# Optimization experiments

Measured on AMD Instinct MI355X. Metric: run time of the kernel, lower is better.

The kernel has to match this reference:

```python
import jax, jax.numpy as jnp
import numpy as np

N_NODES = 100000
LATENT_DIM = 8
SAMPLE_SIZE = 8192
N_EDGES = 1000000
EPS = 1e-6


def setup_inputs() -> dict:
    key = jax.random.key(0)
    k1, k2, k3, k4, k5 = jax.random.split(key, 5)
    latent_Z = jax.random.normal(k1, (N_NODES, LATENT_DIM), dtype=jnp.float32)
    alpha = jax.random.normal(k2, (1,), dtype=jnp.float32)
    sample_idx = jax.random.randint(k3, (SAMPLE_SIZE,), 0, N_NODES, dtype=jnp.int64)
    sparse_sample_i = jax.random.randint(k4, (N_EDGES,), 0, N_NODES, dtype=jnp.int64)
    sparse_sample_j = jax.random.randint(k5, (N_EDGES,), 0, N_NODES, dtype=jnp.int64)
    return {"latent_Z": latent_Z, "alpha": alpha, "sample_idx": sample_idx,
            "sparse_sample_i": sparse_sample_i, "sparse_sample_j": sparse_sample_j}


def reference(latent_Z, alpha, sample_idx, sparse_sample_i, sparse_sample_j):
    # --- dense non-edge term over the sampled subgraph ---
    Zs = latent_Z[sample_idx]                              # [S, D]
    diff = Zs[:, None, :] - Zs[None, :, :] + EPS           # [S, S, D]
    dist = jnp.sqrt(jnp.sum(diff * diff, axis=-1))         # [S, S]
    mat = jnp.exp(-dist)                                   # [S, S]
    # original uses exp(ones) vectors in the matmul-with-ones trick -> factor e^2
    ones_exp_sq = jnp.exp(jnp.float32(1.0)) ** 2
    offdiag_sum = jnp.sum(mat) - jnp.sum(jnp.diagonal(mat))
    z_pdist1 = jnp.exp(alpha[0]) * 0.5 * ones_exp_sq * offdiag_sum
    # --- sparse positive-edge term ---
    ed = latent_Z[sparse_sample_i] - latent_Z[sparse_sample_j] + EPS  # [E, D]
    edist = jnp.sqrt(jnp.sum(ed * ed, axis=-1))                        # [E]
    z_pdist2 = jnp.sum(-edist + alpha[0])
    return z_pdist2 - z_pdist1
```

## Files before the change

kernel.cpp:

```cpp
#include <hip/hip_runtime.h>
#include <hip/hip_bf16.h>
#include <math.h>

#define NNODES   100000
#define S        8192
#define D        8
#define EPSF     1e-6f
#define LOG2E    1.442695040888963f
#define EPS_S    (LOG2E * EPSF)
#define NT2      256

#define ZBS_OFF  0
#define U_OFF    131104
#define V_OFF    163872
#define ZB_OFF   196640
#define BK_OFF   1796736

#define NSBLK    256
#define NDBLK    1024
#define NWPP     32
#define ZROW     8192

typedef __attribute__((ext_vector_type(8)))  short short8_t;
typedef __attribute__((ext_vector_type(16))) float f32x16;

__device__ __forceinline__ float block_reduce_f(float v, float* sm) {
    #pragma unroll
    for (int off = 32; off > 0; off >>= 1) v += __shfl_down(v, off, 64);
    int lane = threadIdx.x & 63, wid = threadIdx.x >> 6;
    if (lane == 0) sm[wid] = v;
    __syncthreads();
    float s = 0.f;
    if (threadIdx.x == 0) {
        for (int w = 0; w < 4; ++w) s += sm[w];
    }
    return s;
}

__global__ __launch_bounds__(256) void gather_kernel(const float* __restrict__ Z,
                                                     const int* __restrict__ idx,
                                                     ushort* __restrict__ zbs,
                                                     float* __restrict__ u,
                                                     float* __restrict__ v,
                                                     ushort* __restrict__ zb16,
                                                     char* __restrict__ buckets) {
    int gid = blockIdx.x * 256 + threadIdx.x;

    if (blockIdx.x == 0 && threadIdx.x < 161) {
        *(double*)(buckets + threadIdx.x * 128) = 0.0;
    }
    if (blockIdx.x == 0 && threadIdx.x == 200) {
        short8_t zz = { 0,0,0,0,0,0,0,0 };
        *(short8_t*)(zbs + (size_t)ZROW * 8) = zz;
    }

    if (gid < S) {
        int n = idx[gid];
        const float4* zp = (const float4*)(Z + (size_t)n * D);
        float4 a = zp[0], b = zp[1];
        float z[8] = { a.x, a.y, a.z, a.w, b.x, b.y, b.z, b.w };
        float ss = 0.f;
        short8_t h;
        #pragma unroll
        for (int k = 0; k < 8; ++k) {
            float zs = LOG2E * z[k];
            __hip_bfloat16 hb = __float2bfloat16(zs);
            float hf = __bfloat162float(hb);
            ss = fmaf(hf, hf, ss);
            h[k] = (short)__builtin_bit_cast(unsigned short, hb);
        }
        *(short8_t*)(zbs + (size_t)gid * 8) = h;
        u[gid] = ss + 8.f * EPS_S * EPS_S;
        v[gid] = ss;
    }

    if (gid < NNODES) {
        const float4* zp = (const float4*)(Z + (size_t)gid * D);
        float4 a = zp[0], b = zp[1];
        float z[8] = { a.x, a.y, a.z, a.w, b.x, b.y, b.z, b.w };
        short8_t o;
        #pragma unroll
        for (int k = 0; k < 8; ++k) {
            __hip_bfloat16 bb = __float2bfloat16(z[k]);
            o[k] = (short)__builtin_bit_cast(unsigned short, bb);
        }
        *(short8_t*)(zb16 + (size_t)gid * 8) = o;
    }
}

#define UNPACK8(u4, f)                                        \
    f[0] = __uint_as_float(u4.x << 16);                       \
    f[1] = __uint_as_float(u4.x & 0xffff0000u);               \
    f[2] = __uint_as_float(u4.y << 16);                       \
    f[3] = __uint_as_float(u4.y & 0xffff0000u);               \
    f[4] = __uint_as_float(u4.z << 16);                       \
    f[5] = __uint_as_float(u4.z & 0xffff0000u);               \
    f[6] = __uint_as_float(u4.w << 16);                       \
    f[7] = __uint_as_float(u4.w & 0xffff0000u);

__device__ __forceinline__ float edge_dist8(const uint4* __restrict__ zb,
                                            int4 ia0, int4 ia1, int4 ib0, int4 ib1) {
    int aidx[8] = { ia0.x, ia0.y, ia0.z, ia0.w, ia1.x, ia1.y, ia1.z, ia1.w };
    int bidx[8] = { ib0.x, ib0.y, ib0.z, ib0.w, ib1.x, ib1.y, ib1.z, ib1.w };
    uint4 ua[8], ub[8];
    #pragma unroll
    for (int q = 0; q < 8; ++q) { ua[q] = zb[aidx[q]]; ub[q] = zb[bidx[q]]; }
    float acc = 0.f;
    #pragma unroll
    for (int q = 0; q < 8; ++q) {
        float fa[8], fb[8];
        UNPACK8(ua[q], fa);
        UNPACK8(ub[q], fb);
        float s2 = 0.f;
        #pragma unroll
        for (int k = 0; k < 8; ++k) {
            float d = fa[k] - fb[k] + EPSF;
            s2 = fmaf(d, d, s2);
        }
        acc += __builtin_amdgcn_sqrtf(s2);
    }
    return acc;
}

__device__ __forceinline__ void dense_sweep32(const ushort* __restrict__ zbs,
                                              const float* __restrict__ v,
                                              short8_t afrag, const float4* u4,
                                              int ti, int tj0, int cnt, int c31, int g,
                                              float& ax, float& ay, float& az, float& aw) {
    const ushort* bp = zbs + (size_t)(g ? ZROW : (tj0 * 32 + c31)) * 8;
    size_t step = g ? 0 : 256;
    const float* vp = v + tj0 * 32 + c31;
    short8_t bnext = *(const short8_t*)bp;
    float    vnext = vp[0];
    #pragma unroll 4
    for (int t = 0; t < cnt; ++t) {
        short8_t bc = bnext;
        float    vtc = vnext;
        if (t + 1 < cnt) {
            bnext = *(const short8_t*)(bp + (size_t)(t + 1) * step);
            vnext = vp[(t + 1) * 32];
        }
        float w = (tj0 + t == ti) ? 1.f : 2.f;
        f32x16 c = { 0.f, 0.f, 0.f, 0.f, 0.f, 0.f, 0.f, 0.f,
                     0.f, 0.f, 0.f, 0.f, 0.f, 0.f, 0.f, 0.f };
        c = __builtin_amdgcn_mfma_f32_32x32x16_bf16(afrag, bc, c, 0, 0, 0);
        #pragma unroll
        for (int q = 0; q < 4; ++q) {
            float s0 = u4[q].x + vtc, s1 = u4[q].y + vtc;
            float s2 = u4[q].z + vtc, s3 = u4[q].w + vtc;
            float d0 = fmaf(c[4*q+0], -2.f, s0);
            float d1 = fmaf(c[4*q+1], -2.f, s1);
            float d2 = fmaf(c[4*q+2], -2.f, s2);
            float d3 = fmaf(c[4*q+3], -2.f, s3);
            ax = fmaf(w, __builtin_amdgcn_exp2f(-__builtin_amdgcn_sqrtf(__builtin_fabsf(d0))), ax);
            ay = fmaf(w, __builtin_amdgcn_exp2f(-__builtin_amdgcn_sqrtf(__builtin_fabsf(d1))), ay);
            az = fmaf(w, __builtin_amdgcn_exp2f(-__builtin_amdgcn_sqrtf(__builtin_fabsf(d2))), az);
            aw = fmaf(w, __builtin_amdgcn_exp2f(-__builtin_amdgcn_sqrtf(__builtin_fabsf(d3))), aw);
        }
    }
}

__global__ __launch_bounds__(256) void fused_kernel(
        const ushort* __restrict__ zbs, const float* __restrict__ u,
        const float* __restrict__ v, const ushort* __restrict__ zb16,
        const int* __restrict__ ei, const int* __restrict__ ej, int ne,
        const float* __restrict__ alpha, char* __restrict__ buckets,
        float* __restrict__ out) {
    __shared__ float red[4];
    __shared__ unsigned composeFlag;
    int tid = threadIdx.x, bx = blockIdx.x;
    float s;

    if (bx < NSBLK) {
        const uint4* zb = (const uint4*)zb16;
        const int4* ei4 = (const int4*)ei;
        const int4* ej4 = (const int4*)ej;
        float acc = 0.f;
        int nchunk = ne >> 3;
        int stride = NSBLK * 256;
        int c = bx * 256 + tid;
        if (c < nchunk) {
            int4 ia0 = ei4[2*c], ia1 = ei4[2*c+1];
            int4 ib0 = ej4[2*c], ib1 = ej4[2*c+1];
            while (true) {
                int cn = c + stride;
                bool more = cn < nchunk;
                int4 na0, na1, nb0, nb1;
                if (more) {
                    na0 = ei4[2*cn]; na1 = ei4[2*cn+1];
                    nb0 = ej4[2*cn]; nb1 = ej4[2*cn+1];
                }
                acc += edge_dist8(zb, ia0, ia1, ib0, ib1);
                if (!more) break;
                ia0 = na0; ia1 = na1; ib0 = nb0; ib1 = nb1; c = cn;
            }
        }
        for (int e = (nchunk << 3) + bx * 256 + tid; e < ne; e += stride) {
            uint4 ua = zb[ei[e]];
            uint4 ub = zb[ej[e]];
            float fa[8], fb[8];
            UNPACK8(ua, fa);
            UNPACK8(ub, fb);
            float s2 = 0.f;
            #pragma unroll
            for (int k = 0; k < 8; ++k) {
                float d = fa[k] - fb[k] + EPSF;
                s2 = fmaf(d, d, s2);
            }
            acc += __builtin_amdgcn_sqrtf(s2);
        }
        s = block_reduce_f(acc, red);
    } else {
        int dbx  = bx - NSBLK;
        int wave = tid >> 6, lane = tid & 63;
        int g = lane >> 5, c31 = lane & 31;

        int p  = dbx >> 3;
        int wv = (dbx & 7) * 4 + wave;
        int k0 = (wv * 257) / NWPP;
        int k1 = ((wv + 1) * 257) / NWPP;
        int n1 = NT2 - p;

        float ax = 0.f, ay = 0.f, az = 0.f, aw = 0.f;

        int eA = k1 < n1 ? k1 : n1;
        if (k0 < eA) {
            int ti = p;
            short8_t afrag = *(const short8_t*)(zbs + (size_t)(ti * 32 + c31) * 8);
            float4 u4[4];
            #pragma unroll
            for (int q = 0; q < 4; ++q) u4[q] = *(const float4*)(u + ti * 32 + 8 * q + 4 * g);
            dense_sweep32(zbs, v, afrag, u4, ti, p + k0, eA - k0, c31, g, ax, ay, az, aw);
        }
        int sB = k0 > n1 ? k0 : n1;
        if (sB < k1) {
            int ti = (NT2 - 1) - p;
            short8_t afrag = *(const short8_t*)(zbs + (size_t)(ti * 32 + c31) * 8);
            float4 u4[4];
            #pragma unroll
            for (int q = 0; q < 4; ++q) u4[q] = *(const float4*)(u + ti * 32 + 8 * q + 4 * g);
            dense_sweep32(zbs, v, afrag, u4, ti, ti + (sB - n1), k1 - sB, c31, g, ax, ay, az, aw);
        }
        s = block_reduce_f((ax + ay) + (az + aw), red);
    }

    double* dbuck = (double*)(buckets);
    double* sbuck = (double*)(buckets + 64 * 128);
    unsigned* gdone = (unsigned*)(buckets + 160 * 128);

    if (tid == 0) {
        int  sparse = (bx < NSBLK);
        int  sid = sparse ? (bx & 15) : ((bx - NSBLK) & 63);
        int  cid = sparse ? (64 + (bx >> 4)) : ((bx - NSBLK) >> 4);
        double* sumslot = sparse ? (double*)((char*)sbuck + sid * 128)
                                 : (double*)((char*)dbuck + sid * 128);
        (void)atomicAdd(sumslot, (double)s);
        __builtin_amdgcn_s_waitcnt(0);
        unsigned oc = atomicAdd((unsigned*)(buckets + (80 + cid) * 128), 1u);
        unsigned g = 0xFFFFu;
        if (oc == 15u) {
            __builtin_amdgcn_s_waitcnt(0);
            g = atomicAdd(gdone, 1u);
        }
        composeFlag = (g == 79u) ? 1u : 0u;
    }
    __syncthreads();

    if (composeFlag) {
        __shared__ double acc2[2];
        int lane = tid & 63, w = tid >> 6;
        double val = 0.0;
        if (w == 0) val = atomicAdd((double*)((char*)dbuck + lane * 128), 0.0);
        else if (w == 1 && lane < 16) val = atomicAdd((double*)((char*)sbuck + lane * 128), 0.0);
        #pragma unroll
        for (int off = 32; off > 0; off >>= 1) val += __shfl_down(val, off, 64);
        if (w == 0 && lane == 0) acc2[0] = val;
        if (w == 1 && lane == 0) acc2[1] = val;
        __syncthreads();
        if (tid == 0) {
            double Dsum = acc2[0], Ssum = acc2[1];
            double trace = (double)S * exp(-sqrt(8.0) * (double)EPSF);
            double offdiag = Dsum - trace;
            double a = (double)alpha[0];
            double z_pdist2 = (double)ne * a - Ssum;
            double z_pdist1 = exp(a) * 0.5 * 7.3890560989306495 * offdiag;
            out[0] = (float)(z_pdist2 - z_pdist1);
        }
    }
}

extern "C" void kernel_launch(void* const* d_in, const int* in_sizes, int n_in,
                              void* d_out, int out_size, void* d_ws, size_t ws_size,
                              hipStream_t stream) {
    const float* latent_Z = (const float*)d_in[0];
    const float* alpha    = (const float*)d_in[1];
    const int*   sidx     = (const int*)d_in[2];
    const int*   ei       = (const int*)d_in[3];
    const int*   ej       = (const int*)d_in[4];
    int ne = in_sizes[3];
    float* out = (float*)d_out;
    char*  ws  = (char*)d_ws;

    ushort* zbs   = (ushort*)(ws + ZBS_OFF);
    float*  u     = (float*)(ws + U_OFF);
    float*  v     = (float*)(ws + V_OFF);
    ushort* zb16  = (ushort*)(ws + ZB_OFF);
    char*   bk    = ws + BK_OFF;

    gather_kernel<<<(NNODES + 255) / 256, 256, 0, stream>>>(latent_Z, sidx,
                                                            zbs, u, v, zb16, bk);
    fused_kernel<<<NSBLK + NDBLK, 256, 0, stream>>>(zbs, u, v, zb16, ei, ej, ne,
                                                    alpha, bk, out);
}
```

Measured before the change: 30.84 us.

## Merge sparse edge work into every dense block instead of dedicated sparse blocks

The dedicated sparse blocks are removed. All 1024 blocks now first process a grid-stride share of the edge list, four edges per thread per iteration, and then run their dense tile sweep. The two partial sums are reduced together and written to per-bucket double accumulators, and the completion counters and bucket layout are resized to match. The goal is to balance memory-bound gather work with exp/sqrt-bound dense work inside each block so that both overlap across the GPU. The cost is fewer loads in flight per thread (4 edges instead of 8, and no software prefetch), plus extra atomics per block.

```diff
diff --git a/kernel.cpp b/kernel.cpp
--- a/kernel.cpp
+++ b/kernel.cpp
@@ -16,7 +16,6 @@
 #define ZB_OFF   196640
 #define BK_OFF   1796736
 
-#define NSBLK    256
 #define NDBLK    1024
 #define NWPP     32
 #define ZROW     8192
@@ -24,17 +23,20 @@
 typedef __attribute__((ext_vector_type(8)))  short short8_t;
 typedef __attribute__((ext_vector_type(16))) float f32x16;
 
-__device__ __forceinline__ float block_reduce_f(float v, float* sm) {
+__device__ __forceinline__ void block_reduce_2(float a, float b, float* sma,
+                                               float* smb, float& ra, float& rb) {
     #pragma unroll
-    for (int off = 32; off > 0; off >>= 1) v += __shfl_down(v, off, 64);
+    for (int off = 32; off > 0; off >>= 1) {
+        a += __shfl_down(a, off, 64);
+        b += __shfl_down(b, off, 64);
+    }
     int lane = threadIdx.x & 63, wid = threadIdx.x >> 6;
-    if (lane == 0) sm[wid] = v;
+    if (lane == 0) { sma[wid] = a; smb[wid] = b; }
     __syncthreads();
-    float s = 0.f;
     if (threadIdx.x == 0) {
-        for (int w = 0; w < 4; ++w) s += sm[w];
-    }
-    return s;
+        ra = 0.f; rb = 0.f;
+        for (int w = 0; w < 4; ++w) { ra += sma[w]; rb += smb[w]; }
+    }
 }
 
 __global__ __launch_bounds__(256) void gather_kernel(const float* __restrict__ Z,
@@ -46,7 +48,7 @@
                                                      char* __restrict__ buckets) {
     int gid = blockIdx.x * 256 + threadIdx.x;
 
-    if (blockIdx.x == 0 && threadIdx.x < 161) {
+    if (blockIdx.x == 0 && threadIdx.x < 193) {
         *(double*)(buckets + threadIdx.x * 128) = 0.0;
     }
     if (blockIdx.x == 0 && threadIdx.x == 200) {
@@ -97,30 +99,6 @@
     f[5] = __uint_as_float(u4.z & 0xffff0000u);               \
     f[6] = __uint_as_float(u4.w << 16);                       \
     f[7] = __uint_as_float(u4.w & 0xffff0000u);
-
-__device__ __forceinline__ float edge_dist8(const uint4* __restrict__ zb,
-                                            int4 ia0, int4 ia1, int4 ib0, int4 ib1) {
-    int aidx[8] = { ia0.x, ia0.y, ia0.z, ia0.w, ia1.x, ia1.y, ia1.z, ia1.w };
-    int bidx[8] = { ib0.x, ib0.y, ib0.z, ib0.w, ib1.x, ib1.y, ib1.z, ib1.w };
-    uint4 ua[8], ub[8];
-    #pragma unroll
-    for (int q = 0; q < 8; ++q) { ua[q] = zb[aidx[q]]; ub[q] = zb[bidx[q]]; }
-    float acc = 0.f;
-    #pragma unroll
-    for (int q = 0; q < 8; ++q) {
-        float fa[8], fb[8];
-        UNPACK8(ua[q], fa);
-        UNPACK8(ub[q], fb);
-        float s2 = 0.f;
-        #pragma unroll
-        for (int k = 0; k < 8; ++k) {
-            float d = fa[k] - fb[k] + EPSF;
-            s2 = fmaf(d, d, s2);
-        }
-        acc += __builtin_amdgcn_sqrtf(s2);
-    }
-    return acc;
-}
 
 __device__ __forceinline__ void dense_sweep32(const ushort* __restrict__ zbs,
                                               const float* __restrict__ v,
@@ -166,36 +144,38 @@
         const int* __restrict__ ei, const int* __restrict__ ej, int ne,
         const float* __restrict__ alpha, char* __restrict__ buckets,
         float* __restrict__ out) {
-    __shared__ float red[4];
+    __shared__ float reda[4], redb[4];
     __shared__ unsigned composeFlag;
     int tid = threadIdx.x, bx = blockIdx.x;
-    float s;
-
-    if (bx < NSBLK) {
+
+    float sacc = 0.f;
+    {
         const uint4* zb = (const uint4*)zb16;
-        const int4* ei4 = (const int4*)ei;
-        const int4* ej4 = (const int4*)ej;
-        float acc = 0.f;
-        int nchunk = ne >> 3;
-        int stride = NSBLK * 256;
-        int c = bx * 256 + tid;
-        if (c < nchunk) {
-            int4 ia0 = ei4[2*c], ia1 = ei4[2*c+1];
-            int4 ib0 = ej4[2*c], ib1 = ej4[2*c+1];
-            while (true) {
-                int cn = c + stride;
-                bool more = cn < nchunk;
-                int4 na0, na1, nb0, nb1;
-                if (more) {
-                    na0 = ei4[2*cn]; na1 = ei4[2*cn+1];
-                    nb0 = ej4[2*cn]; nb1 = ej4[2*cn+1];
+        int nchunk = ne >> 2;
+        int stride = NDBLK * 256;
+        for (int c = bx * 256 + tid; c < nchunk; c += stride) {
+            int4 ia = ((const int4*)ei)[c];
+            int4 ib = ((const int4*)ej)[c];
+            int aidx[4] = { ia.x, ia.y, ia.z, ia.w };
+            int bidx[4] = { ib.x, ib.y, ib.z, ib.w };
+            uint4 ua[4], ub[4];
+            #pragma unroll
+            for (int q = 0; q < 4; ++q) { ua[q] = zb[aidx[q]]; ub[q] = zb[bidx[q]]; }
+            #pragma unroll
+            for (int q = 0; q < 4; ++q) {
+                float fa[8], fb[8];
+                UNPACK8(ua[q], fa);
+                UNPACK8(ub[q], fb);
+                float s2 = 0.f;
+                #pragma unroll
+                for (int k = 0; k < 8; ++k) {
+                    float d = fa[k] - fb[k] + EPSF;
+                    s2 = fmaf(d, d, s2);
                 }
-                acc += edge_dist8(zb, ia0, ia1, ib0, ib1);
-                if (!more) break;
-                ia0 = na0; ia1 = na1; ib0 = nb0; ib1 = nb1; c = cn;
+                sacc += __builtin_amdgcn_sqrtf(s2);
             }
         }
-        for (int e = (nchunk << 3) + bx * 256 + tid; e < ne; e += stride) {
+        for (int e = (nchunk << 2) + bx * 256 + tid; e < ne; e += stride) {
             uint4 ua = zb[ei[e]];
             uint4 ub = zb[ej[e]];
             float fa[8], fb[8];
@@ -207,71 +187,68 @@
                 float d = fa[k] - fb[k] + EPSF;
                 s2 = fmaf(d, d, s2);
             }
-            acc += __builtin_amdgcn_sqrtf(s2);
-        }
-        s = block_reduce_f(acc, red);
-    } else {
-        int dbx  = bx - NSBLK;
-        int wave = tid >> 6, lane = tid & 63;
-        int g = lane >> 5, c31 = lane & 31;
-
-        int p  = dbx >> 3;
-        int wv = (dbx & 7) * 4 + wave;
-        int k0 = (wv * 257) / NWPP;
-        int k1 = ((wv + 1) * 257) / NWPP;
-        int n1 = NT2 - p;
-
-        float ax = 0.f, ay = 0.f, az = 0.f, aw = 0.f;
-
-        int eA = k1 < n1 ? k1 : n1;
-        if (k0 < eA) {
-            int ti = p;
-            short8_t afrag = *(const short8_t*)(zbs + (size_t)(ti * 32 + c31) * 8);
-            float4 u4[4];
-            #pragma unroll
-            for (int q = 0; q < 4; ++q) u4[q] = *(const float4*)(u + ti * 32 + 8 * q + 4 * g);
-            dense_sweep32(zbs, v, afrag, u4, ti, p + k0, eA - k0, c31, g, ax, ay, az, aw);
-        }
-        int sB = k0 > n1 ? k0 : n1;
-        if (sB < k1) {
-            int ti = (NT2 - 1) - p;
-            short8_t afrag = *(const short8_t*)(zbs + (size_t)(ti * 32 + c31) * 8);
-            float4 u4[4];
-            #pragma unroll
-            for (int q = 0; q < 4; ++q) u4[q] = *(const float4*)(u + ti * 32 + 8 * q + 4 * g);
-            dense_sweep32(zbs, v, afrag, u4, ti, ti + (sB - n1), k1 - sB, c31, g, ax, ay, az, aw);
-        }
-        s = block_reduce_f((ax + ay) + (az + aw), red);
-    }
+            sacc += __builtin_amdgcn_sqrtf(s2);
+        }
+    }
+
+    int wave = tid >> 6, lane = tid & 63;
+    int g = lane >> 5, c31 = lane & 31;
+
+    int p  = bx >> 3;
+    int wv = (bx & 7) * 4 + wave;
+    int k0 = (wv * 257) / NWPP;
+    int k1 = ((wv + 1) * 257) / NWPP;
+    int n1 = NT2 - p;
+
+    float ax = 0.f, ay = 0.f, az = 0.f, aw = 0.f;
+
+    int eA = k1 < n1 ? k1 : n1;
+    if (k0 < eA) {
+        int ti = p;
+        short8_t afrag = *(const short8_t*)(zbs + (size_t)(ti * 32 + c31) * 8);
+        float4 u4[4];
+        #pragma unroll
+        for (int q = 0; q < 4; ++q) u4[q] = *(const float4*)(u + ti * 32 + 8 * q + 4 * g);
+        dense_sweep32(zbs, v, afrag, u4, ti, p + k0, eA - k0, c31, g, ax, ay, az, aw);
+    }
+    int sB = k0 > n1 ? k0 : n1;
+    if (sB < k1) {
+        int ti = (NT2 - 1) - p;
+        short8_t afrag = *(const short8_t*)(zbs + (size_t)(ti * 32 + c31) * 8);
+        float4 u4[4];
+        #pragma unroll
+        for (int q = 0; q < 4; ++q) u4[q] = *(const float4*)(u + ti * 32 + 8 * q + 4 * g);
+        dense_sweep32(zbs, v, afrag, u4, ti, ti + (sB - n1), k1 - sB, c31, g, ax, ay, az, aw);
+    }
+
+    float sd = 0.f, ss = 0.f;
+    block_reduce_2((ax + ay) + (az + aw), sacc, reda, redb, sd, ss);
 
     double* dbuck = (double*)(buckets);
     double* sbuck = (double*)(buckets + 64 * 128);
-    unsigned* gdone = (unsigned*)(buckets + 160 * 128);
+    unsigned* gdone = (unsigned*)(buckets + 192 * 128);
 
     if (tid == 0) {
-        int  sparse = (bx < NSBLK);
-        int  sid = sparse ? (bx & 15) : ((bx - NSBLK) & 63);
-        int  cid = sparse ? (64 + (bx >> 4)) : ((bx - NSBLK) >> 4);
-        double* sumslot = sparse ? (double*)((char*)sbuck + sid * 128)
-                                 : (double*)((char*)dbuck + sid * 128);
-        (void)atomicAdd(sumslot, (double)s);
+        int b = bx & 63;
+        (void)atomicAdd((double*)((char*)dbuck + b * 128), (double)sd);
+        (void)atomicAdd((double*)((char*)sbuck + b * 128), (double)ss);
         __builtin_amdgcn_s_waitcnt(0);
-        unsigned oc = atomicAdd((unsigned*)(buckets + (80 + cid) * 128), 1u);
-        unsigned g = 0xFFFFu;
+        unsigned oc = atomicAdd((unsigned*)(buckets + (128 + (bx >> 4)) * 128), 1u);
+        unsigned gg = 0xFFFFu;
         if (oc == 15u) {
             __builtin_amdgcn_s_waitcnt(0);
-            g = atomicAdd(gdone, 1u);
-        }
-        composeFlag = (g == 79u) ? 1u : 0u;
+            gg = atomicAdd(gdone, 1u);
+        }
+        composeFlag = (gg == 63u) ? 1u : 0u;
     }
     __syncthreads();
 
     if (composeFlag) {
         __shared__ double acc2[2];
-        int lane = tid & 63, w = tid >> 6;
+        int w = tid >> 6;
         double val = 0.0;
         if (w == 0) val = atomicAdd((double*)((char*)dbuck + lane * 128), 0.0);
-        else if (w == 1 && lane < 16) val = atomicAdd((double*)((char*)sbuck + lane * 128), 0.0);
+        else if (w == 1) val = atomicAdd((double*)((char*)sbuck + lane * 128), 0.0);
         #pragma unroll
         for (int off = 32; off > 0; off >>= 1) val += __shfl_down(val, off, 64);
         if (w == 0 && lane == 0) acc2[0] = val;
@@ -309,6 +286,6 @@
 
     gather_kernel<<<(NNODES + 255) / 256, 256, 0, stream>>>(latent_Z, sidx,
                                                             zbs, u, v, zb16, bk);
-    fused_kernel<<<NSBLK + NDBLK, 256, 0, stream>>>(zbs, u, v, zb16, ei, ej, ne,
-                                                    alpha, bk, out);
-}
+    fused_kernel<<<NDBLK, 256, 0, stream>>>(zbs, u, v, zb16, ei, ej, ne,
+                                            alpha, bk, out);
+}
```

Result: no change. 30.58 us (-0.8%).
